# Kernel tuning notes

Measured on AMD Instinct MI355X. Metric: run time of the kernel, lower is better.

The kernel has to match this reference:

```python
import jax, jax.numpy as jnp
import numpy as np

BN_EPS = 1e-3          # nn.BatchNorm1d(..., eps=0.001)
NUM_PILLARS = 600000   # M = total occupied pillars across the batch
N_POINTS = 3_000_000
C_IN, C_OUT = 10, 64


def setup_inputs() -> dict:
    key = jax.random.key(0)
    k1, k2, k3 = jax.random.split(key, 3)
    pts_feature = jax.random.normal(k1, (N_POINTS, C_IN), dtype=jnp.float32)
    point_pillar_indices = jax.random.randint(k2, (N_POINTS,), 0, NUM_PILLARS, dtype=jnp.int32)
    # Linear(C_IN, C_OUT, bias=False), kaiming_normal init
    W = jax.random.normal(k3, (C_IN, C_OUT), dtype=jnp.float32) * np.sqrt(2.0 / C_IN)
    # BatchNorm1d in eval mode (running stats)
    gamma = jnp.ones((C_OUT,), jnp.float32)
    beta = jnp.zeros((C_OUT,), jnp.float32)
    run_mean = jnp.zeros((C_OUT,), jnp.float32)
    run_var = jnp.ones((C_OUT,), jnp.float32)
    return {"pts_feature": pts_feature, "point_pillar_indices": point_pillar_indices,
            "W": W, "gamma": gamma, "beta": beta, "run_mean": run_mean, "run_var": run_var}


def reference(pts_feature, point_pillar_indices, W, gamma, beta, run_mean, run_var):
    # shared MLP: Linear(no bias) -> BatchNorm1d(eval) -> ReLU, fused per-point
    h = pts_feature @ W                                        # (N, C_OUT)
    h = gamma * (h - run_mean) * jax.lax.rsqrt(run_var + BN_EPS) + beta
    h = jax.nn.relu(h)
    # scatter_max over irregular pillar ids -> (M, C_OUT)
    pooled = jax.ops.segment_max(h, point_pillar_indices, num_segments=NUM_PILLARS)
    # torch scatter_max leaves empty pillars at 0; jax gives -inf -> replace
    return jnp.where(jnp.isfinite(pooled), pooled, 0.0)
```

## Files before the change

### kernel.cpp

```cpp
#include <hip/hip_runtime.h>
#include <hip/hip_bf16.h>

#define C_IN 10
#define C_OUT 64
#define BN_EPS 1e-3f

#define BP    128
#define CB    256
#define NBMAX 4704
#define TS    2048

typedef __attribute__((ext_vector_type(8))) short bf16x8;
typedef __attribute__((ext_vector_type(4))) float f32x4;


__global__ __launch_bounds__(256) void k1_hist(const int* __restrict__ idx, int n, int chunk,
                                               unsigned* __restrict__ ghist, int NB) {
    __shared__ unsigned h[NBMAX];
    const int b = blockIdx.x, t = threadIdx.x;
    for (int i = t; i < NB; i += 256) h[i] = 0u;
    __syncthreads();
    const int lo = b * chunk;
    const int hi = min(n, lo + chunk);
    for (int i = lo + t; i < hi; i += 256)
        atomicAdd(&h[((unsigned)idx[i]) >> 7], 1u);
    __syncthreads();
    for (int k = t; k < NB; k += 256) ghist[(size_t)k * CB + b] = h[k];
}

__global__ __launch_bounds__(256) void k2a_reduce(const unsigned* __restrict__ g, int G,
                                                  unsigned* __restrict__ tsum) {
    __shared__ unsigned s[256];
    const int t = threadIdx.x;
    const int base = blockIdx.x * TS + t * 8;
    unsigned acc = 0;
#pragma unroll
    for (int j = 0; j < 8; ++j) { int gi = base + j; if (gi < G) acc += g[gi]; }
    s[t] = acc; __syncthreads();
    for (int off = 128; off > 0; off >>= 1) { if (t < off) s[t] += s[t + off]; __syncthreads(); }
    if (t == 0) tsum[blockIdx.x] = s[0];
}

__global__ __launch_bounds__(256) void k2b_scan(unsigned* __restrict__ tsum, int nt) {
    __shared__ unsigned partial[256], basev[256];
    const int t = threadIdx.x;
    const int per = (nt + 255) / 256;
    const int lo = t * per, hi = min(nt, lo + per);
    unsigned s = 0;
    for (int i = lo; i < hi; ++i) s += tsum[i];
    partial[t] = s; __syncthreads();
    if (t == 0) { unsigned a = 0; for (int k = 0; k < 256; ++k) { basev[k] = a; a += partial[k]; } }
    __syncthreads();
    unsigned a = basev[t];
    for (int i = lo; i < hi; ++i) { unsigned v = tsum[i]; tsum[i] = a; a += v; }
}

__global__ __launch_bounds__(256) void k2c_apply(unsigned* __restrict__ g, int G,
                                                 const unsigned* __restrict__ tsum,
                                                 unsigned* __restrict__ bstart, int NB, int n) {
    __shared__ unsigned s[256];
    const int t = threadIdx.x;
    const int base = blockIdx.x * TS + t * 8;
    unsigned v[8]; unsigned acc = 0;
#pragma unroll
    for (int j = 0; j < 8; ++j) { int gi = base + j; v[j] = (gi < G) ? g[gi] : 0u; acc += v[j]; }
    s[t] = acc; __syncthreads();
    for (int off = 1; off < 256; off <<= 1) {
        unsigned x = (t >= off) ? s[t - off] : 0u; __syncthreads();
        s[t] += x; __syncthreads();
    }
    unsigned excl = ((t == 0) ? 0u : s[t - 1]) + tsum[blockIdx.x];
#pragma unroll
    for (int j = 0; j < 8; ++j) {
        int gi = base + j;
        if (gi < G) {
            g[gi] = excl;
            if ((gi & (CB - 1)) == 0) bstart[gi / CB] = excl;
            excl += v[j];
        }
    }
    if (blockIdx.x == 0 && t == 0) bstart[NB] = (unsigned)n;
}

__global__ __launch_bounds__(256) void k3_scatter(const int* __restrict__ idx, int n, int chunk,
                                                  const unsigned* __restrict__ scanned,
                                                  unsigned* __restrict__ rec, int NB) {
    __shared__ unsigned cnt[NBMAX];
    __shared__ unsigned basel[NBMAX];
    const int b = blockIdx.x, t = threadIdx.x;
    for (int k = t; k < NB; k += 256) { basel[k] = scanned[(size_t)k * CB + b]; cnt[k] = 0u; }
    __syncthreads();
    const int lo = b * chunk, hi = min(n, lo + chunk);
    for (int i = lo + t; i < hi; i += 256) {
        unsigned pid = (unsigned)idx[i];
        unsigned k = pid >> 7;
        unsigned r = atomicAdd(&cnt[k], 1u);
        rec[basel[k] + r] = ((pid & 127u) << 22) | (unsigned)i;
    }
}


static __device__ __forceinline__ unsigned pk2(float2 v) {
    __hip_bfloat162 h = __float22bfloat162_rn(v);
    return *reinterpret_cast<unsigned*>(&h);
}

__global__ __launch_bounds__(256) void pool_mfma_kernel(
    const float* __restrict__ pts,
    const unsigned* __restrict__ rec,
    const unsigned* __restrict__ bstart,
    const float* __restrict__ W,
    const float* __restrict__ gamma, const float* __restrict__ beta,
    const float* __restrict__ mean, const float* __restrict__ var,
    float* __restrict__ out, int M)
{
    __shared__ unsigned smax[129 * 64];
    __shared__ unsigned astage[256 * 20];
    __shared__ unsigned char slp[256];

    const int b = blockIdx.x;
    const int t = threadIdx.x;
    const int lane = t & 63;
    const int w = t >> 6;
    const int g  = lane >> 4;
    const int c0 = lane & 15;

    {
        uint4* s4 = (uint4*)smax;
        const uint4 z = make_uint4(0, 0, 0, 0);
        for (int i = t; i < 129 * 16; i += 256) s4[i] = z;
    }

    bf16x8 bfrag[4];
#pragma unroll
    for (int tc = 0; tc < 4; ++tc) {
        const int ch = 16 * tc + c0;
        const float sc = gamma[ch] * rsqrtf(var[ch] + BN_EPS);
        const float sh = fmaf(-mean[ch], sc, beta[ch]);
        union { bf16x8 v; unsigned short u[8]; } B;
#pragma unroll
        for (int j = 0; j < 8; ++j) {
            const int k = g * 8 + j;
            float val = 0.f;
            if (k < 10) val = W[k * C_OUT + ch] * sc;
            else if (k == 10) val = sh;
            __hip_bfloat16 hb = __float2bfloat16(val);
            B.u[j] = *reinterpret_cast<unsigned short*>(&hb);
        }
        bfrag[tc] = B.v;
    }

    const unsigned base = bstart[b];
    const int T = (int)(bstart[b + 1] - base);
    const int nwin = (T + 255) >> 8;

    float2 pf0, pf1, pf2, pf3, pf4;
    unsigned prec = 0; bool have = false;
    if (t < T) {
        prec = rec[base + t];
        const float2* f2 = (const float2*)(pts + (size_t)(prec & 0x3FFFFFu) * C_IN);
        pf0 = f2[0]; pf1 = f2[1]; pf2 = f2[2]; pf3 = f2[3]; pf4 = f2[4];
        have = true;
    }

    for (int k = 0; k < nwin; ++k) {
        __syncthreads();
        {
            uint4* ap = (uint4*)&astage[(unsigned)t * 20];
            const uint4 z = make_uint4(0, 0, 0, 0);
            if (have) {
                slp[t] = (unsigned char)(prec >> 22);
                ap[0] = make_uint4(pk2(pf0), pk2(pf1), pk2(pf2), pk2(pf3));
                ap[1] = make_uint4(pk2(pf4), 0x00003F80u , 0u, 0u);
            } else {
                slp[t] = 128;
                ap[0] = z; ap[1] = z;
            }
            ap[2] = z; ap[3] = z;
        }
        __syncthreads();
        have = false;
        {
            const int nr = (k + 1) * 256 + t;
            if (nr < T) {
                prec = rec[base + nr];
                const float2* f2 = (const float2*)(pts + (size_t)(prec & 0x3FFFFFu) * C_IN);
                pf0 = f2[0]; pf1 = f2[1]; pf2 = f2[2]; pf3 = f2[3]; pf4 = f2[4];
                have = true;
            }
        }
#pragma unroll
        for (int ti = 0; ti < 4; ++ti) {
            const int tbase = (4 * w + ti) * 16;
            union { uint4 q; bf16x8 v; } A;
            A.q = *(const uint4*)&astage[(unsigned)(tbase + c0) * 20 + (unsigned)(g * 4)];
            const f32x4 z4 = {0.f, 0.f, 0.f, 0.f};
            f32x4 a0 = __builtin_amdgcn_mfma_f32_16x16x32_bf16(A.v, bfrag[0], z4, 0, 0, 0);
            f32x4 a1 = __builtin_amdgcn_mfma_f32_16x16x32_bf16(A.v, bfrag[1], z4, 0, 0, 0);
            f32x4 a2 = __builtin_amdgcn_mfma_f32_16x16x32_bf16(A.v, bfrag[2], z4, 0, 0, 0);
            f32x4 a3 = __builtin_amdgcn_mfma_f32_16x16x32_bf16(A.v, bfrag[3], z4, 0, 0, 0);
#pragma unroll
            for (int r = 0; r < 4; ++r) {
                const int pt = tbase + g * 4 + r;
                const unsigned lp = slp[pt];
                unsigned* srow = &smax[lp * 64 + c0];
                atomicMax(&srow[0],  __float_as_uint(fmaxf(a0[r], 0.f)));
                atomicMax(&srow[16], __float_as_uint(fmaxf(a1[r], 0.f)));
                atomicMax(&srow[32], __float_as_uint(fmaxf(a2[r], 0.f)));
                atomicMax(&srow[48], __float_as_uint(fmaxf(a3[r], 0.f)));
            }
        }
    }
    __syncthreads();

    const uint4* s4 = (const uint4*)smax;
    float4* o4 = (float4*)out;
    const size_t base4 = (size_t)b * (BP * C_OUT / 4);
    const size_t tot4  = (size_t)M * (C_OUT / 4);
    for (int i = t; i < BP * C_OUT / 4; i += 256) {
        size_t gi = base4 + (size_t)i;
        if (gi < tot4) {
            uint4 v = s4[i];
            o4[gi] = *reinterpret_cast<float4*>(&v);
        }
    }
}

#define CHUNK 256
#define FSTRIDE 11

__global__ __launch_bounds__(256) void zero_u32_kernel(unsigned* __restrict__ p, int n) {
    int i = blockIdx.x * 256 + threadIdx.x;
    int s = gridDim.x * 256;
    for (; i < n; i += s) p[i] = 0u;
}

__global__ __launch_bounds__(256) void hist_kernel(const int* __restrict__ idx, int n,
                                                   unsigned* __restrict__ hist, int nb) {
    __shared__ unsigned h[NBMAX];
    for (int i = threadIdx.x; i < nb; i += 256) h[i] = 0u;
    __syncthreads();
    int stride = gridDim.x * 256;
    for (int i = blockIdx.x * 256 + threadIdx.x; i < n; i += stride)
        atomicAdd(&h[((unsigned)idx[i]) >> 7], 1u);
    __syncthreads();
    for (int i = threadIdx.x; i < nb; i += 256) {
        unsigned v = h[i];
        if (v) atomicAdd(&hist[i], v);
    }
}

__global__ __launch_bounds__(256) void scan_kernel(const unsigned* __restrict__ hist,
                                                   unsigned* __restrict__ cursor, int nb) {
    __shared__ unsigned partial[256];
    __shared__ unsigned base[256];
    int per = (nb + 255) / 256;
    int lo = threadIdx.x * per;
    int hi = lo + per; if (hi > nb) hi = nb;
    unsigned s = 0;
    for (int i = lo; i < hi; ++i) s += hist[i];
    partial[threadIdx.x] = s;
    __syncthreads();
    if (threadIdx.x == 0) {
        unsigned acc = 0;
        for (int t = 0; t < 256; ++t) { base[t] = acc; acc += partial[t]; }
    }
    __syncthreads();
    unsigned acc = base[threadIdx.x];
    for (int i = lo; i < hi; ++i) { cursor[i] = acc; acc += hist[i]; }
}

__global__ __launch_bounds__(256) void scatter_ids_kernel(const int* __restrict__ idx, int n,
                                                          unsigned* __restrict__ cursor,
                                                          unsigned* __restrict__ rec) {
    int stride = gridDim.x * 256;
    for (int i = blockIdx.x * 256 + threadIdx.x; i < n; i += stride) {
        unsigned pid = (unsigned)idx[i];
        unsigned pos = atomicAdd(&cursor[pid >> 7], 1u);
        rec[pos] = ((pid & (BP - 1)) << 22) | (unsigned)i;
    }
}

__global__ __launch_bounds__(256) void pool_kernel(
    const float* __restrict__ pts, const unsigned* __restrict__ rec,
    const unsigned* __restrict__ cursor, const float* __restrict__ W,
    const float* __restrict__ gamma, const float* __restrict__ beta,
    const float* __restrict__ mean, const float* __restrict__ var,
    float* __restrict__ out, int M)
{
    __shared__ unsigned smax[BP * C_OUT];
    __shared__ float    feat[CHUNK * FSTRIDE];
    __shared__ unsigned slp[CHUNK];
    const int b = blockIdx.x, t = threadIdx.x;
    const int lane = t & 63, wid = t >> 6;
    for (int i = t; i < BP * C_OUT; i += 256) smax[i] = 0u;
    float w[C_IN];
#pragma unroll
    for (int j = 0; j < C_IN; ++j) w[j] = W[j * C_OUT + lane];
    const float scale = gamma[lane] * rsqrtf(var[lane] + BN_EPS);
    const float shift = fmaf(-mean[lane], scale, beta[lane]);
    const unsigned start = (b == 0) ? 0u : cursor[b - 1];
    const int total = (int)(cursor[b] - start);
    float fr[C_IN]; unsigned rcr = 0; bool hav = false;
    if (t < total) {
        rcr = rec[start + t];
        const float2* f2 = (const float2*)(pts + (size_t)(rcr & 0x3FFFFFu) * C_IN);
#pragma unroll
        for (int j = 0; j < 5; ++j) { float2 v = f2[j]; fr[2*j] = v.x; fr[2*j+1] = v.y; }
        hav = true;
    }
    for (int chunk = 0; chunk < total; chunk += CHUNK) {
        const int nrec = min(CHUNK, total - chunk);
        __syncthreads();
        if (hav) {
            slp[t] = rcr >> 22;
#pragma unroll
            for (int j = 0; j < C_IN; ++j) feat[t * FSTRIDE + j] = fr[j];
        }
        __syncthreads();
        const int nr = chunk + CHUNK + t;
        hav = false;
        if (nr < total) {
            rcr = rec[start + nr];
            const float2* f2 = (const float2*)(pts + (size_t)(rcr & 0x3FFFFFu) * C_IN);
#pragma unroll
            for (int j = 0; j < 5; ++j) { float2 v = f2[j]; fr[2*j] = v.x; fr[2*j+1] = v.y; }
            hav = true;
        }
        for (int i = wid; i < nrec; i += 4) {
            const unsigned lp = slp[i];
            const float* f = &feat[i * FSTRIDE];
            float h = 0.f;
#pragma unroll
            for (int j = 0; j < C_IN; ++j) h = fmaf(f[j], w[j], h);
            h = fmaxf(fmaf(h, scale, shift), 0.f);
            atomicMax(&smax[(lp << 6) + lane], __float_as_uint(h));
        }
    }
    __syncthreads();
    const float4* s4 = (const float4*)smax;
    float4* o4 = (float4*)out;
    const size_t base4 = (size_t)b * (BP * C_OUT / 4);
    const size_t tot4  = (size_t)M * (C_OUT / 4);
    for (int i = t; i < BP * C_OUT / 4; i += 256) {
        size_t g = base4 + (size_t)i;
        if (g < tot4) o4[g] = s4[i];
    }
}

__global__ __launch_bounds__(256) void zero_out_kernel(float4* __restrict__ out4, int n4) {
    int i = blockIdx.x * blockDim.x + threadIdx.x;
    int stride = gridDim.x * blockDim.x;
    float4 z = make_float4(0.f, 0.f, 0.f, 0.f);
    for (int j = i; j < n4; j += stride) out4[j] = z;
}

__global__ __launch_bounds__(256) void pillar_scatter_kernel(
    const float* __restrict__ pts, const int* __restrict__ idx,
    const float* __restrict__ W, const float* __restrict__ gamma,
    const float* __restrict__ beta, const float* __restrict__ mean,
    const float* __restrict__ var, unsigned int* __restrict__ out, int npoints)
{
    const int lane = threadIdx.x & 63;
    float w[C_IN];
#pragma unroll
    for (int j = 0; j < C_IN; ++j) w[j] = W[j * C_OUT + lane];
    const float scale = gamma[lane] * rsqrtf(var[lane] + BN_EPS);
    const float shift = fmaf(-mean[lane], scale, beta[lane]);
    const int wave_id = (blockIdx.x * blockDim.x + threadIdx.x) >> 6;
    const int nwaves  = (gridDim.x * blockDim.x) >> 6;
    for (int p = wave_id; p < npoints; p += nwaves) {
        const float* f = pts + (size_t)p * C_IN;
        float h = 0.f;
#pragma unroll
        for (int j = 0; j < C_IN; ++j) h = fmaf(f[j], w[j], h);
        h = fmaxf(fmaf(h, scale, shift), 0.f);
        atomicMax(&out[(size_t)idx[p] * C_OUT + lane], __float_as_uint(h));
    }
}


extern "C" void kernel_launch(void* const* d_in, const int* in_sizes, int n_in,
                              void* d_out, int out_size, void* d_ws, size_t ws_size,
                              hipStream_t stream) {
    const float* pts   = (const float*)d_in[0];
    const int*   idx   = (const int*)  d_in[1];
    const float* W     = (const float*)d_in[2];
    const float* gamma = (const float*)d_in[3];
    const float* beta  = (const float*)d_in[4];
    const float* mean  = (const float*)d_in[5];
    const float* var   = (const float*)d_in[6];

    const int npoints = in_sizes[0] / C_IN;
    const int M       = out_size / C_OUT;
    const int NB      = (M + BP - 1) / BP;
    const int G       = NB * CB;
    const int nt      = (G + TS - 1) / TS;
    const int chunk   = (npoints + CB - 1) / CB;

    const size_t rec_off = (((size_t)G + (size_t)nt + (size_t)NB + 1) + 63) & ~(size_t)63;
    const size_t need    = (rec_off + (size_t)npoints) * sizeof(unsigned);

    if (NB <= NBMAX && npoints < (1 << 22) && nt <= 65535 && ws_size >= need) {
        unsigned* ghist  = (unsigned*)d_ws;
        unsigned* tsum   = ghist + G;
        unsigned* bstart = tsum + nt;
        unsigned* rec    = (unsigned*)d_ws + rec_off;

        k1_hist          <<<CB, 256, 0, stream>>>(idx, npoints, chunk, ghist, NB);
        k2a_reduce       <<<nt, 256, 0, stream>>>(ghist, G, tsum);
        k2b_scan         <<<1,  256, 0, stream>>>(tsum, nt);
        k2c_apply        <<<nt, 256, 0, stream>>>(ghist, G, tsum, bstart, NB, npoints);
        k3_scatter       <<<CB, 256, 0, stream>>>(idx, npoints, chunk, ghist, rec, NB);
        pool_mfma_kernel <<<NB, 256, 0, stream>>>(pts, rec, bstart, W, gamma, beta,
                                                  mean, var, (float*)d_out, M);
        return;
    }

    const size_t rec_off_f1 = ((size_t)(2 * NB) + 63) & ~(size_t)63;
    const size_t need_f1    = (rec_off_f1 + (size_t)npoints) * sizeof(unsigned);
    if (NB <= NBMAX && npoints < (1 << 22) && ws_size >= need_f1) {
        unsigned* cursor = (unsigned*)d_ws;
        unsigned* hist   = cursor + NB;
        unsigned* rec    = (unsigned*)d_ws + rec_off_f1;
        zero_u32_kernel<<<(2 * NB + 255) / 256, 256, 0, stream>>>(cursor, 2 * NB);
        hist_kernel<<<256, 256, 0, stream>>>(idx, npoints, hist, NB);
        scan_kernel<<<1, 256, 0, stream>>>(hist, cursor, NB);
        scatter_ids_kernel<<<2048, 256, 0, stream>>>(idx, npoints, cursor, rec);
        pool_kernel<<<NB, 256, 0, stream>>>(pts, rec, cursor, W, gamma, beta, mean, var,
                                            (float*)d_out, M);
        return;
    }

    zero_out_kernel<<<2048, 256, 0, stream>>>((float4*)d_out, out_size / 4);
    pillar_scatter_kernel<<<2048, 256, 0, stream>>>(
        pts, idx, W, gamma, beta, mean, var, (unsigned int*)d_out, npoints);
}
```

Before: 219.4 us.

## Replace LDS staging with wave shuffles and swizzle shared max rows

```diff
diff --git a/kernel.cpp b/kernel.cpp
--- a/kernel.cpp
+++ b/kernel.cpp
@@ -105,7 +105,7 @@
     return *reinterpret_cast<unsigned*>(&h);
 }
 
-__global__ __launch_bounds__(256) void pool_mfma_kernel(
+__global__ __launch_bounds__(256) void pool_mfma2_kernel(
     const float* __restrict__ pts,
     const unsigned* __restrict__ rec,
     const unsigned* __restrict__ bstart,
@@ -114,22 +114,15 @@
     const float* __restrict__ mean, const float* __restrict__ var,
     float* __restrict__ out, int M)
 {
-    __shared__ unsigned smax[129 * 64];
-    __shared__ unsigned astage[256 * 20];
-    __shared__ unsigned char slp[256];
-
-    const int b = blockIdx.x;
-    const int t = threadIdx.x;
-    const int lane = t & 63;
-    const int w = t >> 6;
-    const int g  = lane >> 4;
-    const int c0 = lane & 15;
-
-    {
-        uint4* s4 = (uint4*)smax;
-        const uint4 z = make_uint4(0, 0, 0, 0);
-        for (int i = t; i < 129 * 16; i += 256) s4[i] = z;
-    }
+    __shared__ unsigned smax[BP * C_OUT];
+
+    const int b = blockIdx.x, t = threadIdx.x;
+    const int lane = t & 63, w = t >> 6;
+    const int g = lane >> 4, c0 = lane & 15;
+
+    uint4* s4 = (uint4*)smax;
+    const uint4 zq = make_uint4(0u, 0u, 0u, 0u);
+    for (int i = t; i < BP * C_OUT / 4; i += 256) s4[i] = zq;
 
     bf16x8 bfrag[4];
 #pragma unroll
@@ -152,76 +145,81 @@
 
     const unsigned base = bstart[b];
     const int T = (int)(bstart[b + 1] - base);
-    const int nwin = (T + 255) >> 8;
+
+    __syncthreads();
 
     float2 pf0, pf1, pf2, pf3, pf4;
-    unsigned prec = 0; bool have = false;
-    if (t < T) {
-        prec = rec[base + t];
-        const float2* f2 = (const float2*)(pts + (size_t)(prec & 0x3FFFFFu) * C_IN);
+    unsigned rc = 0u;
+    if (w * 64 < T) {
+        const int i = min(w * 64 + lane, T - 1);
+        rc = rec[base + i];
+        const float2* f2 = (const float2*)(pts + (size_t)(rc & 0x3FFFFFu) * C_IN);
         pf0 = f2[0]; pf1 = f2[1]; pf2 = f2[2]; pf3 = f2[3]; pf4 = f2[4];
-        have = true;
-    }
-
-    for (int k = 0; k < nwin; ++k) {
-        __syncthreads();
-        {
-            uint4* ap = (uint4*)&astage[(unsigned)t * 20];
-            const uint4 z = make_uint4(0, 0, 0, 0);
-            if (have) {
-                slp[t] = (unsigned char)(prec >> 22);
-                ap[0] = make_uint4(pk2(pf0), pk2(pf1), pk2(pf2), pk2(pf3));
-                ap[1] = make_uint4(pk2(pf4), 0x00003F80u , 0u, 0u);
-            } else {
-                slp[t] = 128;
-                ap[0] = z; ap[1] = z;
-            }
-            ap[2] = z; ap[3] = z;
-        }
-        __syncthreads();
-        have = false;
-        {
-            const int nr = (k + 1) * 256 + t;
-            if (nr < T) {
-                prec = rec[base + nr];
-                const float2* f2 = (const float2*)(pts + (size_t)(prec & 0x3FFFFFu) * C_IN);
-                pf0 = f2[0]; pf1 = f2[1]; pf2 = f2[2]; pf3 = f2[3]; pf4 = f2[4];
-                have = true;
-            }
-        }
+    }
+
+    for (int k = 0; w * 64 + k * 256 < T; ++k) {
+        const unsigned p0 = pk2(pf0), p1 = pk2(pf1), p2 = pk2(pf2),
+                       p3 = pk2(pf3), p4 = pk2(pf4);
+        const int lpv = (int)(rc >> 22);
+
+        const int nb_ = w * 64 + (k + 1) * 256;
+        if (nb_ < T) {
+            const int i = min(nb_ + lane, T - 1);
+            rc = rec[base + i];
+            const float2* f2 = (const float2*)(pts + (size_t)(rc & 0x3FFFFFu) * C_IN);
+            pf0 = f2[0]; pf1 = f2[1]; pf2 = f2[2]; pf3 = f2[3]; pf4 = f2[4];
+        }
+
 #pragma unroll
         for (int ti = 0; ti < 4; ++ti) {
-            const int tbase = (4 * w + ti) * 16;
+            const int srcA = ti * 16 + c0;
+            const unsigned s0 = (unsigned)__shfl((int)p0, srcA);
+            const unsigned s1 = (unsigned)__shfl((int)p1, srcA);
+            const unsigned s2 = (unsigned)__shfl((int)p2, srcA);
+            const unsigned s3 = (unsigned)__shfl((int)p3, srcA);
+            const unsigned s4v = (unsigned)__shfl((int)p4, srcA);
             union { uint4 q; bf16x8 v; } A;
-            A.q = *(const uint4*)&astage[(unsigned)(tbase + c0) * 20 + (unsigned)(g * 4)];
+            if (g == 0)      A.q = make_uint4(s0, s1, s2, s3);
+            else if (g == 1) A.q = make_uint4(s4v, 0x00003F80u, 0u, 0u);
+            else             A.q = make_uint4(0u, 0u, 0u, 0u);
+
             const f32x4 z4 = {0.f, 0.f, 0.f, 0.f};
             f32x4 a0 = __builtin_amdgcn_mfma_f32_16x16x32_bf16(A.v, bfrag[0], z4, 0, 0, 0);
             f32x4 a1 = __builtin_amdgcn_mfma_f32_16x16x32_bf16(A.v, bfrag[1], z4, 0, 0, 0);
             f32x4 a2 = __builtin_amdgcn_mfma_f32_16x16x32_bf16(A.v, bfrag[2], z4, 0, 0, 0);
             f32x4 a3 = __builtin_amdgcn_mfma_f32_16x16x32_bf16(A.v, bfrag[3], z4, 0, 0, 0);
-#pragma unroll
-            for (int r = 0; r < 4; ++r) {
-                const int pt = tbase + g * 4 + r;
-                const unsigned lp = slp[pt];
-                unsigned* srow = &smax[lp * 64 + c0];
-                atomicMax(&srow[0],  __float_as_uint(fmaxf(a0[r], 0.f)));
-                atomicMax(&srow[16], __float_as_uint(fmaxf(a1[r], 0.f)));
-                atomicMax(&srow[32], __float_as_uint(fmaxf(a2[r], 0.f)));
-                atomicMax(&srow[48], __float_as_uint(fmaxf(a3[r], 0.f)));
-            }
-        }
-    }
-    __syncthreads();
-
-    const uint4* s4 = (const uint4*)smax;
-    float4* o4 = (float4*)out;
-    const size_t base4 = (size_t)b * (BP * C_OUT / 4);
-    const size_t tot4  = (size_t)M * (C_OUT / 4);
-    for (int i = t; i < BP * C_OUT / 4; i += 256) {
-        size_t gi = base4 + (size_t)i;
-        if (gi < tot4) {
-            uint4 v = s4[i];
-            o4[gi] = *reinterpret_cast<float4*>(&v);
+
+            const int sb = ti * 16 + g * 4;
+            const int l0 = __shfl(lpv, sb + 0);
+            const int l1 = __shfl(lpv, sb + 1);
+            const int l2 = __shfl(lpv, sb + 2);
+            const int l3 = __shfl(lpv, sb + 3);
+
+#define CONSUME_R(LP, R) { \
+            unsigned* rowp = &smax[((unsigned)(LP)) << 6]; \
+            const unsigned rb = (unsigned)(c0 + ((LP) << 2)); \
+            atomicMax(&rowp[(rb +  0u) & 63u], __float_as_uint(fmaxf(a0[R], 0.f))); \
+            atomicMax(&rowp[(rb + 16u) & 63u], __float_as_uint(fmaxf(a1[R], 0.f))); \
+            atomicMax(&rowp[(rb + 32u) & 63u], __float_as_uint(fmaxf(a2[R], 0.f))); \
+            atomicMax(&rowp[(rb + 48u) & 63u], __float_as_uint(fmaxf(a3[R], 0.f))); }
+            CONSUME_R(l0, 0); CONSUME_R(l1, 1); CONSUME_R(l2, 2); CONSUME_R(l3, 3);
+#undef CONSUME_R
+        }
+    }
+    __syncthreads();
+
+    const int row = t >> 1;
+    const int half = t & 1;
+    const int gp = b * BP + row;
+    if (gp < M) {
+        float4* o4 = (float4*)out;
+        const size_t ob = (size_t)gp * (C_OUT / 4);
+#pragma unroll
+        for (int j = 0; j < 8; ++j) {
+            const int q = half * 8 + j;
+            uint4 v = s4[row * 16 + q];
+            const int oq = (q - row) & 15;
+            o4[ob + oq] = *reinterpret_cast<float4*>(&v);
         }
     }
 }
@@ -338,13 +336,13 @@
         }
     }
     __syncthreads();
-    const float4* s4 = (const float4*)smax;
+    const float4* sf4 = (const float4*)smax;
     float4* o4 = (float4*)out;
     const size_t base4 = (size_t)b * (BP * C_OUT / 4);
     const size_t tot4  = (size_t)M * (C_OUT / 4);
     for (int i = t; i < BP * C_OUT / 4; i += 256) {
-        size_t g = base4 + (size_t)i;
-        if (g < tot4) o4[g] = s4[i];
+        size_t gq = base4 + (size_t)i;
+        if (gq < tot4) o4[gq] = sf4[i];
     }
 }
 
@@ -407,13 +405,13 @@
         unsigned* bstart = tsum + nt;
         unsigned* rec    = (unsigned*)d_ws + rec_off;
 
-        k1_hist          <<<CB, 256, 0, stream>>>(idx, npoints, chunk, ghist, NB);
-        k2a_reduce       <<<nt, 256, 0, stream>>>(ghist, G, tsum);
-        k2b_scan         <<<1,  256, 0, stream>>>(tsum, nt);
-        k2c_apply        <<<nt, 256, 0, stream>>>(ghist, G, tsum, bstart, NB, npoints);
-        k3_scatter       <<<CB, 256, 0, stream>>>(idx, npoints, chunk, ghist, rec, NB);
-        pool_mfma_kernel <<<NB, 256, 0, stream>>>(pts, rec, bstart, W, gamma, beta,
-                                                  mean, var, (float*)d_out, M);
+        k1_hist           <<<CB, 256, 0, stream>>>(idx, npoints, chunk, ghist, NB);
+        k2a_reduce        <<<nt, 256, 0, stream>>>(ghist, G, tsum);
+        k2b_scan          <<<1,  256, 0, stream>>>(tsum, nt);
+        k2c_apply         <<<nt, 256, 0, stream>>>(ghist, G, tsum, bstart, NB, npoints);
+        k3_scatter        <<<CB, 256, 0, stream>>>(idx, npoints, chunk, ghist, rec, NB);
+        pool_mfma2_kernel <<<NB, 256, 0, stream>>>(pts, rec, bstart, W, gamma, beta,
+                                                   mean, var, (float*)d_out, M);
         return;
     }
 
```

Result: faster. 210.8 us (-3.9%).
